# Kernel tuning notes

Hardware: AMD Instinct MI355X
Metric: run time of the kernel (lower is better)

The kernel has to match this reference:

```python
import jax, jax.numpy as jnp
import numpy as np

D_MODEL = 1024
NUM_HEADS = 16
HEAD_DIM = D_MODEL // NUM_HEADS


def setup_inputs() -> dict:
    key = jax.random.key(0)
    ks = jax.random.split(key, 9)
    s = 1.0 / np.sqrt(D_MODEL)
    x = jax.random.normal(ks[0], (2, 2048, D_MODEL), dtype=jnp.float32)
    Wq = jax.random.normal(ks[1], (D_MODEL, D_MODEL), dtype=jnp.float32) * s
    bq = jnp.zeros((D_MODEL,), dtype=jnp.float32)
    Wk = jax.random.normal(ks[2], (D_MODEL, D_MODEL), dtype=jnp.float32) * s
    bk = jnp.zeros((D_MODEL,), dtype=jnp.float32)
    Wv = jax.random.normal(ks[3], (D_MODEL, D_MODEL), dtype=jnp.float32) * s
    bv = jnp.zeros((D_MODEL,), dtype=jnp.float32)
    Wo = jax.random.normal(ks[4], (D_MODEL, D_MODEL), dtype=jnp.float32) * s
    bo = jnp.zeros((D_MODEL,), dtype=jnp.float32)
    return {"x": x, "Wq": Wq, "bq": bq, "Wk": Wk, "bk": bk,
            "Wv": Wv, "bv": bv, "Wo": Wo, "bo": bo}


def reference(x, Wq, bq, Wk, bk, Wv, bv, Wo, bo):
    B, S, D = x.shape
    H, Hd = NUM_HEADS, HEAD_DIM
    scale = 1.0 / np.sqrt(Hd)

    def split_heads(t):  # [B,S,D] -> [B,H,S,Hd]
        return t.reshape(B, S, H, Hd).transpose(0, 2, 1, 3)

    q = split_heads(x @ Wq + bq)
    k = split_heads(x @ Wk + bk)
    v = split_heads(x @ Wv + bv)

    scores = jnp.einsum('bhqd,bhkd->bhqk', q, k) * scale
    scores = scores - jnp.max(scores, axis=-1, keepdims=True)
    attn = jax.nn.softmax(scores, axis=-1)
    attended = jnp.einsum('bhqk,bhkd->bhqd', attn, v)
    attended = attended.transpose(0, 2, 1, 3).reshape(B, S, D)
    return attended @ Wo + bo
```

## Files before the change

kernel.cpp:

```cpp
#include <hip/hip_runtime.h>
#include <hip/hip_bf16.h>

typedef __bf16 bf16_t;
typedef __bf16 bf16x8 __attribute__((ext_vector_type(8)));
typedef __bf16 bf16x4 __attribute__((ext_vector_type(4)));
typedef float floatx4 __attribute__((ext_vector_type(4)));
typedef short short4v __attribute__((ext_vector_type(4)));

#define D_MODEL 1024
#define SEQ     2048
#define BATCH   2
#define NHEAD   16
#define HDIM    64
#define MTOT    (BATCH * SEQ)

#define QSCALE  0.18033688011112042f

union PBu { bf16x4 b; short4v s; };

__device__ __forceinline__ void async_copy16(const bf16_t* g, bf16_t* l) {
    __builtin_amdgcn_global_load_lds(
        (const __attribute__((address_space(1))) void*)g,
        (__attribute__((address_space(3))) void*)l, 16, 0, 0);
}

__global__ void prep_kernel(
    const float* __restrict__ x, bf16_t* __restrict__ xb,
    const float* __restrict__ W0, const float* __restrict__ W1,
    const float* __restrict__ W2, const float* __restrict__ W3,
    bf16_t* __restrict__ T0, bf16_t* __restrict__ T1,
    bf16_t* __restrict__ T2, bf16_t* __restrict__ T3)
{
    const int z = blockIdx.z;
    const int tx = threadIdx.x, ty = threadIdx.y;
    if (z == 4) {
        const int lin = (blockIdx.y * 32 + blockIdx.x) * 256 + ty * 32 + tx;
        const int base = lin * 16;
#pragma unroll
        for (int c = 0; c < 4; ++c) {
            const float4 v = *(const float4*)(x + base + c * 4);
            bf16x4 o = { (bf16_t)v.x, (bf16_t)v.y, (bf16_t)v.z, (bf16_t)v.w };
            *(bf16x4*)(xb + base + c * 4) = o;
        }
        return;
    }
    __shared__ float tile[32][33];
    const float* W = (z == 0) ? W0 : (z == 1) ? W1 : (z == 2) ? W2 : W3;
    bf16_t*     Wt = (z == 0) ? T0 : (z == 1) ? T1 : (z == 2) ? T2 : T3;
    const int k0 = blockIdx.y * 32, n0 = blockIdx.x * 32;
#pragma unroll
    for (int j = 0; j < 32; j += 8)
        tile[ty + j][tx] = W[(size_t)(k0 + ty + j) * D_MODEL + n0 + tx];
    __syncthreads();
#pragma unroll
    for (int j = 0; j < 32; j += 8)
        Wt[(size_t)(n0 + ty + j) * D_MODEL + k0 + tx] = (bf16_t)tile[tx][ty + j];
}

__device__ __forceinline__ void gemm_mainloop(
    const bf16_t* __restrict__ A, const bf16_t* __restrict__ Bt,
    int m0, int n0, bf16_t* As, bf16_t* Bs, floatx4 acc[4][4])
{
    const int tid  = threadIdx.x;
    const int lane = tid & 63;
    const int wid  = tid >> 6;
    const int quad = lane >> 4;
    const int col  = lane & 15;
    const int wm   = (wid >> 1) * 64;
    const int wn   = (wid & 1) * 64;
    const int srow = tid >> 3;
    const int scc  = ((tid & 7) ^ (srow & 7)) * 8;
    const int xorc = col & 7;

    const bf16_t* Ag = A  + (size_t)(m0 + srow) * D_MODEL + scc;
    const bf16_t* Bg = Bt + (size_t)(n0 + srow) * D_MODEL + scc;
    bf16_t* Al = As + tid * 8;
    bf16_t* Bl = Bs + tid * 8;

    for (int kb = 0; kb < D_MODEL; kb += 64) {
#pragma unroll
        for (int p = 0; p < 4; ++p) {
            async_copy16(Ag + kb + p * (32 * D_MODEL), Al + p * 2048);
            async_copy16(Bg + kb + p * (32 * D_MODEL), Bl + p * 2048);
        }
        __syncthreads();
#pragma unroll
        for (int kh = 0; kh < 2; ++kh) {
            bf16x8 af[4], bfr[4];
#pragma unroll
            for (int i = 0; i < 4; ++i)
                af[i] = *(const bf16x8*)(As + (wm + i * 16 + col) * 64 + (((kh * 4 + quad) ^ xorc) * 8));
#pragma unroll
            for (int j = 0; j < 4; ++j)
                bfr[j] = *(const bf16x8*)(Bs + (wn + j * 16 + col) * 64 + (((kh * 4 + quad) ^ xorc) * 8));
#pragma unroll
            for (int i = 0; i < 4; ++i)
#pragma unroll
                for (int j = 0; j < 4; ++j)
                    acc[i][j] = __builtin_amdgcn_mfma_f32_16x16x32_bf16(af[i], bfr[j], acc[i][j], 0, 0, 0);
        }
        __syncthreads();
    }
}

__global__ __launch_bounds__(256, 3) void gemm_qkv(
    const bf16_t* __restrict__ xb,
    const bf16_t* __restrict__ Wtq, const bf16_t* __restrict__ Wtk, const bf16_t* __restrict__ Wtv,
    const float* __restrict__ bq, const float* __restrict__ bk, const float* __restrict__ bv,
    bf16_t* __restrict__ Q, bf16_t* __restrict__ Kh, bf16_t* __restrict__ Vt)
{
    __shared__ bf16_t As[128 * 64];
    __shared__ bf16_t Bs[128 * 64];
    const int z = blockIdx.z;
    const bf16_t* Bt   = (z == 0) ? Wtq : (z == 1) ? Wtk : Wtv;
    const float*  bias = (z == 0) ? bq  : (z == 1) ? bk  : bv;
    bf16_t*       O    = (z == 0) ? Q   : (z == 1) ? Kh  : Vt;
    const float   qs   = (z == 0) ? QSCALE : 1.0f;
    const int m0 = blockIdx.y * 128;
    const int n0 = blockIdx.x * 128;

    floatx4 acc[4][4];
#pragma unroll
    for (int i = 0; i < 4; ++i)
#pragma unroll
        for (int j = 0; j < 4; ++j)
            acc[i][j] = (floatx4){0.f, 0.f, 0.f, 0.f};

    gemm_mainloop(xb, Bt, m0, n0, As, Bs, acc);

    const int tid  = threadIdx.x;
    const int lane = tid & 63;
    const int wid  = tid >> 6;
    const int quad = lane >> 4;
    const int col  = lane & 15;
    const int wm   = (wid >> 1) * 64;
    const int wn   = (wid & 1) * 64;

    if (z == 2) {
#pragma unroll
        for (int i = 0; i < 4; ++i) {
#pragma unroll
            for (int j = 0; j < 4; ++j) {
                const int n = n0 + wn + j * 16 + col;
                const float bb = bias[n];
                const int mb = m0 + wm + i * 16 + quad * 4;
                const size_t bhb = (size_t)((mb >> 11) * NHEAD + (n >> 6)) * (SEQ * HDIM);
                bf16x4 pk = { (bf16_t)(acc[i][j][0] + bb), (bf16_t)(acc[i][j][1] + bb),
                              (bf16_t)(acc[i][j][2] + bb), (bf16_t)(acc[i][j][3] + bb) };
                *(bf16x4*)(O + bhb + (size_t)(n & 63) * SEQ + (mb & 2047)) = pk;
            }
        }
    } else {
#pragma unroll
        for (int i = 0; i < 4; ++i) {
#pragma unroll
            for (int j = 0; j < 4; ++j) {
                const int n = n0 + wn + j * 16 + col;
                const float bb = bias[n];
#pragma unroll
                for (int r = 0; r < 4; ++r) {
                    const int m = m0 + wm + i * 16 + quad * 4 + r;
                    const float v = (acc[i][j][r] + bb) * qs;
                    const size_t bhb = (size_t)((m >> 11) * NHEAD + (n >> 6)) * (SEQ * HDIM);
                    O[bhb + (size_t)(m & 2047) * HDIM + (n & 63)] = (bf16_t)v;
                }
            }
        }
    }
}

__global__ __launch_bounds__(128, 4) void attn_kernel(
    const bf16_t* __restrict__ Q, const bf16_t* __restrict__ K,
    const bf16_t* __restrict__ Vt, bf16_t* __restrict__ A2)
{
    __shared__ bf16_t Ks[64 * 64];
    __shared__ bf16_t Vs[64 * 64];

    const int tid  = threadIdx.x;
    const int lane = tid & 63;
    const int wid  = tid >> 6;
    const int quad = lane >> 4;
    const int col  = lane & 15;
    const int xorc = col & 7;

    const int blk = blockIdx.x;
    const int idx = blk >> 3;
    const int bh  = (blk & 7) * 4 + (idx >> 5);
    const int q0  = (idx & 31) * 64;
    const int b   = bh >> 4, h = bh & 15;

    const bf16_t* Qb = Q  + (size_t)bh * (SEQ * HDIM);
    const bf16_t* Kb = K  + (size_t)bh * (SEQ * HDIM);
    const bf16_t* Vb = Vt + (size_t)bh * (SEQ * HDIM);

    bf16x8 qf[2][2];
#pragma unroll
    for (int st = 0; st < 2; ++st) {
        const int qrow = q0 + wid * 32 + st * 16 + col;
        qf[st][0] = *(const bf16x8*)(Qb + (size_t)qrow * HDIM + quad * 8);
        qf[st][1] = *(const bf16x8*)(Qb + (size_t)qrow * HDIM + 32 + quad * 8);
    }

    floatx4 o_acc[2][4];
    float lsum[2] = {0.f, 0.f};
#pragma unroll
    for (int st = 0; st < 2; ++st)
#pragma unroll
        for (int dt = 0; dt < 4; ++dt)
            o_acc[st][dt] = (floatx4){0.f, 0.f, 0.f, 0.f};

    const int srow = tid >> 3;
    const int scc  = ((tid & 7) ^ (srow & 7)) * 8;
    const bf16_t* Kg = Kb + (size_t)srow * HDIM + scc;
    const bf16_t* Vg = Vb + (size_t)srow * SEQ + scc;
    bf16_t* KsL = Ks + tid * 8;
    bf16_t* VsL = Vs + tid * 8;

    for (int it = 0; it < 32; ++it) {
        const int ko = it * 64;
#pragma unroll
        for (int p = 0; p < 4; ++p) {
            async_copy16(Kg + (size_t)(ko + p * 16) * HDIM, KsL + p * 1024);
            async_copy16(Vg + (size_t)(p * 16) * SEQ + ko, VsL + p * 1024);
        }
        __syncthreads();

        bf16x8 kf[4][2];
#pragma unroll
        for (int t = 0; t < 4; ++t) {
            kf[t][0] = *(const bf16x8*)(Ks + (t * 16 + col) * 64 + ((quad ^ xorc) * 8));
            kf[t][1] = *(const bf16x8*)(Ks + (t * 16 + col) * 64 + (((4 + quad) ^ xorc) * 8));
        }
        short4v vfr[4][4];
#pragma unroll
        for (int dt = 0; dt < 4; ++dt)
#pragma unroll
            for (int t = 0; t < 4; ++t) {
                const int sch = t * 2 + (quad >> 1);
                vfr[dt][t] = *(const short4v*)(Vs + (dt * 16 + col) * 64 + ((sch ^ xorc) * 8) + (quad & 1) * 4);
            }

#pragma unroll
        for (int st = 0; st < 2; ++st) {
            floatx4 s_acc[4];
            short4v pb[4];
#pragma unroll
            for (int t = 0; t < 4; ++t) {
                s_acc[t] = (floatx4){0.f, 0.f, 0.f, 0.f};
                s_acc[t] = __builtin_amdgcn_mfma_f32_16x16x32_bf16(kf[t][0], qf[st][0], s_acc[t], 0, 0, 0);
                s_acc[t] = __builtin_amdgcn_mfma_f32_16x16x32_bf16(kf[t][1], qf[st][1], s_acc[t], 0, 0, 0);
            }
#pragma unroll
            for (int t = 0; t < 4; ++t) {
                const float p0 = __builtin_amdgcn_exp2f(s_acc[t][0]);
                const float p1 = __builtin_amdgcn_exp2f(s_acc[t][1]);
                const float p2 = __builtin_amdgcn_exp2f(s_acc[t][2]);
                const float p3 = __builtin_amdgcn_exp2f(s_acc[t][3]);
                lsum[st] += (p0 + p1) + (p2 + p3);
                PBu u;
                u.b = (bf16x4){ (bf16_t)p0, (bf16_t)p1, (bf16_t)p2, (bf16_t)p3 };
                pb[t] = u.s;
            }
#pragma unroll
            for (int dt = 0; dt < 4; ++dt)
#pragma unroll
                for (int t = 0; t < 4; ++t)
                    o_acc[st][dt] = __builtin_amdgcn_mfma_f32_16x16x16bf16_1k(vfr[dt][t], pb[t], o_acc[st][dt], 0, 0, 0);
        }
        __syncthreads();
    }

#pragma unroll
    for (int st = 0; st < 2; ++st) {
        lsum[st] += __shfl_xor(lsum[st], 16, 64);
        lsum[st] += __shfl_xor(lsum[st], 32, 64);
    }

#pragma unroll
    for (int st = 0; st < 2; ++st) {
        const float inv = 1.0f / lsum[st];
        const int qrow = q0 + wid * 32 + st * 16 + col;
        bf16_t* dst = A2 + ((size_t)(b * SEQ + qrow)) * D_MODEL + h * HDIM + quad * 4;
#pragma unroll
        for (int dt = 0; dt < 4; ++dt) {
            bf16x4 pk = { (bf16_t)(o_acc[st][dt][0] * inv), (bf16_t)(o_acc[st][dt][1] * inv),
                          (bf16_t)(o_acc[st][dt][2] * inv), (bf16_t)(o_acc[st][dt][3] * inv) };
            *(bf16x4*)(dst + dt * 16) = pk;
        }
    }
}

__global__ __launch_bounds__(256, 3) void gemm_proj(
    const bf16_t* __restrict__ A2, const bf16_t* __restrict__ Wto,
    const float* __restrict__ bo, float* __restrict__ out)
{
    __shared__ bf16_t As[64 * 64];
    __shared__ bf16_t Bs[128 * 64];
    const int m0 = blockIdx.y * 64;
    const int n0 = blockIdx.x * 128;

    const int tid  = threadIdx.x;
    const int lane = tid & 63;
    const int wid  = tid >> 6;
    const int quad = lane >> 4;
    const int col  = lane & 15;
    const int wm   = (wid >> 1) * 32;
    const int wn   = (wid & 1) * 64;
    const int srow = tid >> 3;
    const int scc  = ((tid & 7) ^ (srow & 7)) * 8;
    const int xorc = col & 7;

    floatx4 acc[2][4];
#pragma unroll
    for (int i = 0; i < 2; ++i)
#pragma unroll
        for (int j = 0; j < 4; ++j)
            acc[i][j] = (floatx4){0.f, 0.f, 0.f, 0.f};

    const bf16_t* Ag = A2  + (size_t)(m0 + srow) * D_MODEL + scc;
    const bf16_t* Bg = Wto + (size_t)(n0 + srow) * D_MODEL + scc;
    bf16_t* Al = As + tid * 8;
    bf16_t* Bl = Bs + tid * 8;

    for (int kb = 0; kb < D_MODEL; kb += 64) {
#pragma unroll
        for (int p = 0; p < 2; ++p)
            async_copy16(Ag + kb + p * (32 * D_MODEL), Al + p * 2048);
#pragma unroll
        for (int p = 0; p < 4; ++p)
            async_copy16(Bg + kb + p * (32 * D_MODEL), Bl + p * 2048);
        __syncthreads();
#pragma unroll
        for (int kh = 0; kh < 2; ++kh) {
            bf16x8 af[2], bfr[4];
#pragma unroll
            for (int i = 0; i < 2; ++i)
                af[i] = *(const bf16x8*)(As + (wm + i * 16 + col) * 64 + (((kh * 4 + quad) ^ xorc) * 8));
#pragma unroll
            for (int j = 0; j < 4; ++j)
                bfr[j] = *(const bf16x8*)(Bs + (wn + j * 16 + col) * 64 + (((kh * 4 + quad) ^ xorc) * 8));
#pragma unroll
            for (int i = 0; i < 2; ++i)
#pragma unroll
                for (int j = 0; j < 4; ++j)
                    acc[i][j] = __builtin_amdgcn_mfma_f32_16x16x32_bf16(af[i], bfr[j], acc[i][j], 0, 0, 0);
        }
        __syncthreads();
    }

#pragma unroll
    for (int i = 0; i < 2; ++i) {
#pragma unroll
        for (int j = 0; j < 4; ++j) {
            const int n = n0 + wn + j * 16 + col;
            const float bb = bo[n];
#pragma unroll
            for (int r = 0; r < 4; ++r) {
                const int m = m0 + wm + i * 16 + quad * 4 + r;
                out[(size_t)m * D_MODEL + n] = acc[i][j][r] + bb;
            }
        }
    }
}

extern "C" void kernel_launch(void* const* d_in, const int* in_sizes, int n_in,
                              void* d_out, int out_size, void* d_ws, size_t ws_size,
                              hipStream_t stream) {
    const float* x  = (const float*)d_in[0];
    const float* Wq = (const float*)d_in[1];
    const float* bq = (const float*)d_in[2];
    const float* Wk = (const float*)d_in[3];
    const float* bk = (const float*)d_in[4];
    const float* Wv = (const float*)d_in[5];
    const float* bv = (const float*)d_in[6];
    const float* Wo = (const float*)d_in[7];
    const float* bo = (const float*)d_in[8];
    float* out = (float*)d_out;

    const size_t MB = 1ull << 20;
    char* ws = (char*)d_ws;
    bf16_t* Q     = (bf16_t*)(ws + 0 * MB);
    bf16_t* Kh    = (bf16_t*)(ws + 8 * MB);
    bf16_t* Vt    = (bf16_t*)(ws + 16 * MB);
    bf16_t* A2    = (bf16_t*)(ws + 24 * MB);
    bf16_t* xb    = (bf16_t*)(ws + 32 * MB);
    bf16_t* Wtq   = (bf16_t*)(ws + 40 * MB);
    bf16_t* Wtk   = (bf16_t*)(ws + 42 * MB);
    bf16_t* Wtv   = (bf16_t*)(ws + 44 * MB);
    bf16_t* Wto   = (bf16_t*)(ws + 46 * MB);

    prep_kernel<<<dim3(32, 32, 5), dim3(32, 8), 0, stream>>>(
        x, xb, Wq, Wk, Wv, Wo, Wtq, Wtk, Wtv, Wto);

    gemm_qkv<<<dim3(D_MODEL / 128, MTOT / 128, 3), 256, 0, stream>>>(
        xb, Wtq, Wtk, Wtv, bq, bk, bv, Q, Kh, Vt);

    attn_kernel<<<dim3(1024), 128, 0, stream>>>(Q, Kh, Vt, A2);

    gemm_proj<<<dim3(D_MODEL / 128, MTOT / 64), 256, 0, stream>>>(A2, Wto, bo, out);
}
```

Before: 190.9 us.

## Split attention over two KV halves and merge partials in a combine kernel

Attention now splits the key/value sequence into two halves, doubling the grid from 1024 to 2048 blocks, each covering 16 KV tiles instead of 32. Each half writes a normalized partial output and its row sum, and a new combine kernel blends the two with weights l0/(l0+l1) and l1/(l0+l1) into the head-interleaved layout. The row-sum reduction moves from per-lane adds plus shuffles to an extra MFMA against a ones vector. The goal is more parallelism and occupancy on the many compute units. The cost is an extra kernel launch, writing and re-reading the partial outputs, and partials rounded to bf16 before merging.

```diff
diff --git a/kernel.cpp b/kernel.cpp
--- a/kernel.cpp
+++ b/kernel.cpp
@@ -13,6 +13,7 @@
 #define NHEAD   16
 #define HDIM    64
 #define MTOT    (BATCH * SEQ)
+#define LROWS   (32 * 2048)
 
 #define QSCALE  0.18033688011112042f
 
@@ -171,7 +172,7 @@
 
 __global__ __launch_bounds__(128, 4) void attn_kernel(
     const bf16_t* __restrict__ Q, const bf16_t* __restrict__ K,
-    const bf16_t* __restrict__ Vt, bf16_t* __restrict__ A2)
+    const bf16_t* __restrict__ Vt, bf16_t* __restrict__ Opart, float* __restrict__ lpart)
 {
     __shared__ bf16_t Ks[64 * 64];
     __shared__ bf16_t Vs[64 * 64];
@@ -185,9 +186,10 @@
 
     const int blk = blockIdx.x;
     const int idx = blk >> 3;
-    const int bh  = (blk & 7) * 4 + (idx >> 5);
-    const int q0  = (idx & 31) * 64;
-    const int b   = bh >> 4, h = bh & 15;
+    const int bh  = (blk & 7) * 4 + (idx >> 6);
+    const int rem = idx & 63;
+    const int sp  = rem >> 5;
+    const int q0  = (rem & 31) * 64;
 
     const bf16_t* Qb = Q  + (size_t)bh * (SEQ * HDIM);
     const bf16_t* Kb = K  + (size_t)bh * (SEQ * HDIM);
@@ -202,21 +204,24 @@
     }
 
     floatx4 o_acc[2][4];
-    float lsum[2] = {0.f, 0.f};
-#pragma unroll
-    for (int st = 0; st < 2; ++st)
+    floatx4 l_acc[2];
+#pragma unroll
+    for (int st = 0; st < 2; ++st) {
+        l_acc[st] = (floatx4){0.f, 0.f, 0.f, 0.f};
 #pragma unroll
         for (int dt = 0; dt < 4; ++dt)
             o_acc[st][dt] = (floatx4){0.f, 0.f, 0.f, 0.f};
+    }
+    const short4v ones = { (short)0x3F80, (short)0x3F80, (short)0x3F80, (short)0x3F80 };
 
     const int srow = tid >> 3;
     const int scc  = ((tid & 7) ^ (srow & 7)) * 8;
-    const bf16_t* Kg = Kb + (size_t)srow * HDIM + scc;
-    const bf16_t* Vg = Vb + (size_t)srow * SEQ + scc;
+    const bf16_t* Kg = Kb + (size_t)(sp * 1024 + srow) * HDIM + scc;
+    const bf16_t* Vg = Vb + (size_t)srow * SEQ + sp * 1024 + scc;
     bf16_t* KsL = Ks + tid * 8;
     bf16_t* VsL = Vs + tid * 8;
 
-    for (int it = 0; it < 32; ++it) {
+    for (int it = 0; it < 16; ++it) {
         const int ko = it * 64;
 #pragma unroll
         for (int p = 0; p < 4; ++p) {
@@ -256,10 +261,10 @@
                 const float p1 = __builtin_amdgcn_exp2f(s_acc[t][1]);
                 const float p2 = __builtin_amdgcn_exp2f(s_acc[t][2]);
                 const float p3 = __builtin_amdgcn_exp2f(s_acc[t][3]);
-                lsum[st] += (p0 + p1) + (p2 + p3);
                 PBu u;
                 u.b = (bf16x4){ (bf16_t)p0, (bf16_t)p1, (bf16_t)p2, (bf16_t)p3 };
                 pb[t] = u.s;
+                l_acc[st] = __builtin_amdgcn_mfma_f32_16x16x16bf16_1k(ones, pb[t], l_acc[st], 0, 0, 0);
             }
 #pragma unroll
             for (int dt = 0; dt < 4; ++dt)
@@ -272,21 +277,47 @@
 
 #pragma unroll
     for (int st = 0; st < 2; ++st) {
-        lsum[st] += __shfl_xor(lsum[st], 16, 64);
-        lsum[st] += __shfl_xor(lsum[st], 32, 64);
-    }
-
-#pragma unroll
-    for (int st = 0; st < 2; ++st) {
-        const float inv = 1.0f / lsum[st];
+        const float lsum = l_acc[st][0];
+        const float inv  = 1.0f / lsum;
         const int qrow = q0 + wid * 32 + st * 16 + col;
-        bf16_t* dst = A2 + ((size_t)(b * SEQ + qrow)) * D_MODEL + h * HDIM + quad * 4;
+        bf16_t* od = Opart + ((size_t)(sp * 32 + bh) * SEQ + qrow) * HDIM + quad * 4;
 #pragma unroll
         for (int dt = 0; dt < 4; ++dt) {
             bf16x4 pk = { (bf16_t)(o_acc[st][dt][0] * inv), (bf16_t)(o_acc[st][dt][1] * inv),
                           (bf16_t)(o_acc[st][dt][2] * inv), (bf16_t)(o_acc[st][dt][3] * inv) };
-            *(bf16x4*)(dst + dt * 16) = pk;
-        }
+            *(bf16x4*)(od + dt * 16) = pk;
+        }
+        if (quad == 0)
+            lpart[(size_t)sp * LROWS + (size_t)bh * SEQ + qrow] = lsum;
+    }
+}
+
+__global__ __launch_bounds__(256) void attn_combine(
+    const bf16_t* __restrict__ Op, const float* __restrict__ lp, bf16_t* __restrict__ A2)
+{
+    const int tid = threadIdx.x;
+    const int bh  = blockIdx.y;
+    const int q   = blockIdx.x * 64 + (tid >> 2);
+    const int dc  = (tid & 3) * 16;
+    const int b   = bh >> 4, h = bh & 15;
+
+    const float l0 = lp[(size_t)bh * SEQ + q];
+    const float l1 = lp[LROWS + (size_t)bh * SEQ + q];
+    const float rs = 1.0f / (l0 + l1);
+    const float w0 = l0 * rs, w1 = l1 * rs;
+
+    const size_t b0 = ((size_t)bh * SEQ + q) * HDIM + dc;
+    const size_t b1 = ((size_t)(32 + bh) * SEQ + q) * HDIM + dc;
+    bf16_t* dst = A2 + ((size_t)(b * SEQ + q)) * D_MODEL + h * HDIM + dc;
+#pragma unroll
+    for (int c = 0; c < 2; ++c) {
+        const bf16x8 a = *(const bf16x8*)(Op + b0 + c * 8);
+        const bf16x8 d = *(const bf16x8*)(Op + b1 + c * 8);
+        bf16x8 o;
+#pragma unroll
+        for (int j = 0; j < 8; ++j)
+            o[j] = (bf16_t)(w0 * (float)a[j] + w1 * (float)d[j]);
+        *(bf16x8*)(dst + c * 8) = o;
     }
 }
 
@@ -384,10 +415,12 @@
     bf16_t* Vt    = (bf16_t*)(ws + 16 * MB);
     bf16_t* A2    = (bf16_t*)(ws + 24 * MB);
     bf16_t* xb    = (bf16_t*)(ws + 32 * MB);
+    float*  lpart = (float*)(ws + 32 * MB);
     bf16_t* Wtq   = (bf16_t*)(ws + 40 * MB);
     bf16_t* Wtk   = (bf16_t*)(ws + 42 * MB);
     bf16_t* Wtv   = (bf16_t*)(ws + 44 * MB);
     bf16_t* Wto   = (bf16_t*)(ws + 46 * MB);
+    bf16_t* Opart = (bf16_t*)(ws + 48 * MB);
 
     prep_kernel<<<dim3(32, 32, 5), dim3(32, 8), 0, stream>>>(
         x, xb, Wq, Wk, Wv, Wo, Wtq, Wtk, Wtv, Wto);
@@ -395,7 +428,9 @@
     gemm_qkv<<<dim3(D_MODEL / 128, MTOT / 128, 3), 256, 0, stream>>>(
         xb, Wtq, Wtk, Wtv, bq, bk, bv, Q, Kh, Vt);
 
-    attn_kernel<<<dim3(1024), 128, 0, stream>>>(Q, Kh, Vt, A2);
+    attn_kernel<<<dim3(2048), 128, 0, stream>>>(Q, Kh, Vt, Opart, lpart);
+
+    attn_combine<<<dim3(SEQ / 64, BATCH * NHEAD), 256, 0, stream>>>(Opart, lpart, A2);
 
     gemm_proj<<<dim3(D_MODEL / 128, MTOT / 64), 256, 0, stream>>>(A2, Wto, bo, out);
 }
```

Result: no change. 191.8 us (+0.5%).
